# Performance work log

Hardware: AMD Instinct MI355X
Metric: run time of the kernel (lower is better)

Reference implementation:

```python
import jax, jax.numpy as jnp
import numpy as np

BS, NQ, NCLS = 16, 128, 3
T, P = 480, 72          # total targets, points per curve
COST_CLASS_W = 1.0
CURVES_W = 1.0
LOWER_W = 1.0
UPPER_W = 1.0


def setup_inputs() -> dict:
    key = jax.random.key(0)
    k1, k2, k3, k4, k5, k6, k7 = jax.random.split(key, 7)
    pred_logits = jax.random.normal(k1, (BS, NQ, NCLS), dtype=jnp.float32)
    pred_curves = jax.random.uniform(k2, (BS, NQ, 8), dtype=jnp.float32)
    # targets: [T, 5 + 2P] = [class_id, lower_y, upper_y, lower_x, upper_x, xs(P), ys(P)]
    ids = jax.random.randint(k3, (T,), 0, NCLS).astype(jnp.float32)
    ends = jax.random.uniform(k4, (T, 4), dtype=jnp.float32)  # ly, uy, lx, ux
    xs = jax.random.uniform(k5, (T, P), dtype=jnp.float32)
    ys = jax.random.uniform(k6, (T, P), dtype=jnp.float32)
    # variable number of valid points per lane; invalid points marked x = -1
    counts = jax.random.randint(k7, (T,), P // 2, P + 1)
    valid = jnp.arange(P)[None, :] < counts[:, None]
    xs = jnp.where(valid, xs, -1.0)
    targets = jnp.concatenate([ids[:, None], ends, xs, ys], axis=1)
    return {"pred_logits": pred_logits, "pred_curves": pred_curves, "targets": targets}


def reference(pred_logits, pred_curves, targets):
    bs, nq, _ = pred_logits.shape
    BN = bs * nq
    out_prob = jax.nn.softmax(pred_logits.reshape(BN, -1), axis=-1)
    tgt_ids = targets[:, 0].astype(jnp.int32)
    cost_class = -out_prob[:, tgt_ids]                      # [BN, T]

    ob = pred_curves.reshape(BN, 8)
    ly, uy, lx, ux = targets[:, 1], targets[:, 2], targets[:, 3], targets[:, 4]
    # L1 cdist on scalars == abs diff; averaged over (y, x) endpoint coords
    cost_lower = 0.5 * (jnp.abs(ob[:, 0:1] - ly[None, :]) + jnp.abs(ob[:, 2:3] - lx[None, :]))
    cost_upper = 0.5 * (jnp.abs(ob[:, 1:2] - uy[None, :]) + jnp.abs(ob[:, 3:4] - ux[None, :]))

    p = (targets.shape[1] - 5) // 2
    txs = targets[:, 5:5 + p]                               # [T, P]
    tys = targets[:, 5 + p:]                                # [T, P]
    valid = txs >= 0                                        # [T, P]
    per = jnp.sum(valid, axis=1).astype(jnp.float32)        # [T]
    total = jnp.sum(valid).astype(jnp.float32)
    w = jnp.sqrt(total / per)
    w = w / jnp.max(w)                                      # [T]

    p1 = jnp.stack([lx, ly], axis=-1)                       # [T, 2]
    p2 = jnp.stack([ux, uy], axis=-1)
    d = p2 - p1                                             # [T, 2]
    pi = jnp.stack([txs, tys], axis=-1)                     # [T, P, 2]
    p1pi = pi - p1[:, None, :]
    dot = jnp.einsum('tk,tpk->tp', d, p1pi)                 # [T, P]
    nrm = jnp.sqrt(jnp.sum(d * d, axis=-1))                 # [T]
    # original: proj = dot / nrm, then lam = proj / nrm
    lam = (dot / nrm[:, None]) / nrm[:, None]               # [T, P]

    a3, a2 = ob[:, 4], ob[:, 5]
    a1 = ob[:, 3] - a3 - a2 - ob[:, 2]
    a0 = ob[:, 2]
    b3, b2 = ob[:, 6], ob[:, 7]
    b1 = ob[:, 1] - b3 - b2 - ob[:, 0]
    b0 = ob[:, 0]

    L = lam[:, :, None]                                     # [T, P, 1] broadcast vs [BN]
    L2 = L * L
    L3 = L2 * L
    ox = a3 * L3 + a2 * L2 + a1 * L + a0                    # [T, P, BN]
    oy = b3 * L3 + b2 * L2 + b1 * L + b0

    diff = (txs[:, :, None] - ox) ** 2 + (tys[:, :, None] - oy) ** 2
    cost_polys = jnp.sum(jnp.where(valid[:, :, None], diff, 0.0), axis=1)  # [T, BN]
    cost_polys = cost_polys.T * w[None, :]                  # [BN, T]

    C = (COST_CLASS_W * cost_class + CURVES_W * cost_polys / 10.0
         + LOWER_W * cost_lower + UPPER_W * cost_upper)
    return C.reshape(bs, nq, -1)
```

## Files before the change

### kernel.cpp

```cpp
#include <hip/hip_runtime.h>
#include <math.h>

#define BS   16
#define NQ   128
#define NCLS 3
#define T    480
#define P    72
#define BN   (BS * NQ)
#define TROW (5 + 2 * P)
#define BNB  4

#define MD_OFF_B 0
#define EF_OFF_B 61440

__global__ __launch_bounds__(64) void moments_kernel(const float* __restrict__ targets,
                                                     double* __restrict__ MD,
                                                     float* __restrict__ EF) {
    int t    = blockIdx.x;
    int lane = threadIdx.x;
    const float* row = targets + (size_t)t * TROW;
    float ly = row[1], uy = row[2], lx = row[3], ux = row[4];
    float dx = ux - lx, dy = uy - ly;
    float nrm = sqrtf(dx * dx + dy * dy);

    double v[17];
#pragma unroll
    for (int i = 0; i < 17; ++i) v[i] = 0.0;

    for (int p = lane; p < P; p += 64) {
        float tx = row[5 + p];
        float ty = row[5 + P + p];
        if (tx >= 0.0f) {
            float lamf = dx * (tx - lx) + dy * (ty - ly);
            lamf = lamf / nrm / nrm;
            double L   = (double)lamf;
            double txd = (double)tx, tyd = (double)ty;
            double lp = 1.0;
#pragma unroll
            for (int j = 0; j < 7; ++j) {
                v[j] += lp;
                if (j < 4) {
                    v[7 + j]  += txd * lp;
                    v[11 + j] += tyd * lp;
                }
                lp *= L;
            }
            v[15] += txd * txd + tyd * tyd;
            v[16] += 1.0;
        }
    }

#pragma unroll
    for (int off = 32; off > 0; off >>= 1) {
#pragma unroll
        for (int i = 0; i < 17; ++i) v[i] += __shfl_down(v[i], off);
    }

    if (lane == 0) {
#pragma unroll
        for (int j = 0; j < 7; ++j) MD[j * T + t] = v[j];
#pragma unroll
        for (int k = 0; k < 4; ++k) {
            MD[(7 + k) * T + t]  = -2.0 * v[7 + k];
            MD[(11 + k) * T + t] = -2.0 * v[11 + k];
        }
        MD[15 * T + t] = v[15];
        EF[0 * T + t] = ly;
        EF[1 * T + t] = uy;
        EF[2 * T + t] = lx;
        EF[3 * T + t] = ux;
        EF[4 * T + t] = (float)v[16];
        EF[5 * T + t] = row[0];
    }
}

__global__ __launch_bounds__(512) void cost_kernel(const float* __restrict__ logits,
                                                   const float* __restrict__ curves,
                                                   const double* __restrict__ MD,
                                                   const float* __restrict__ EF,
                                                   float* __restrict__ out) {
    __shared__ float wavemin[8];
    int t    = threadIdx.x;
    int bn0  = blockIdx.x * BNB;
    int lane = t & 63;
    int wid  = t >> 6;

    float per = (t < T) ? EF[4 * T + t] : 1e30f;
    float pm = per;
#pragma unroll
    for (int off = 32; off > 0; off >>= 1) pm = fminf(pm, __shfl_xor(pm, off));
    if (lane == 0) wavemin[wid] = pm;
    __syncthreads();
    float per_min = wavemin[0];
#pragma unroll
    for (int i = 1; i < 8; ++i) per_min = fminf(per_min, wavemin[i]);

    if (t >= T) return;
    float w = sqrtf(per_min / per);

    double m[16];
#pragma unroll
    for (int r = 0; r < 16; ++r) m[r] = MD[r * T + t];
    float ly = EF[0 * T + t], uy = EF[1 * T + t];
    float lx = EF[2 * T + t], ux = EF[3 * T + t];
    int   id = (int)EF[5 * T + t];

#pragma unroll
    for (int j = 0; j < BNB; ++j) {
        int bn = bn0 + j;
        const float* ob = curves + (size_t)bn * 8;
        float o0 = ob[0], o1 = ob[1], o2 = ob[2], o3 = ob[3];
        float o4 = ob[4], o5 = ob[5], o6 = ob[6], o7 = ob[7];
        float a0 = o2, a1 = o3 - o4 - o5 - o2, a2 = o5, a3 = o4;
        float b0 = o0, b1 = o1 - o6 - o7 - o0, b2 = o7, b3 = o6;

        double A0 = a0, A1 = a1, A2 = a2, A3 = a3;
        double B0 = b0, B1 = b1, B2 = b2, B3 = b3;
        double acc = m[15]
            + (A0 * A0 + B0 * B0) * m[0]
            + 2.0 * (A0 * A1 + B0 * B1) * m[1]
            + (2.0 * (A0 * A2 + B0 * B2) + A1 * A1 + B1 * B1) * m[2]
            + 2.0 * (A0 * A3 + A1 * A2 + B0 * B3 + B1 * B2) * m[3]
            + (2.0 * (A1 * A3 + B1 * B3) + A2 * A2 + B2 * B2) * m[4]
            + 2.0 * (A2 * A3 + B2 * B3) * m[5]
            + (A3 * A3 + B3 * B3) * m[6]
            + A0 * m[7]  + A1 * m[8]  + A2 * m[9]  + A3 * m[10]
            + B0 * m[11] + B1 * m[12] + B2 * m[13] + B3 * m[14];

        const float* lg = logits + (size_t)bn * NCLS;
        float l0 = lg[0], l1 = lg[1], l2 = lg[2];
        float mx = fmaxf(l0, fmaxf(l1, l2));
        float e0 = __expf(l0 - mx), e1 = __expf(l1 - mx), e2 = __expf(l2 - mx);
        float inv = 1.0f / (e0 + e1 + e2);
        float prob = (id == 0) ? e0 * inv : ((id == 1) ? e1 * inv : e2 * inv);

        float cp = (float)acc * w * 0.1f;
        float cl = 0.5f * (fabsf(b0 - ly) + fabsf(a0 - lx));
        float cu = 0.5f * (fabsf(o1 - uy) + fabsf(o3 - ux));
        out[(size_t)bn * T + t] = -prob + cp + cl + cu;
    }
}

extern "C" void kernel_launch(void* const* d_in, const int* in_sizes, int n_in,
                              void* d_out, int out_size, void* d_ws, size_t ws_size,
                              hipStream_t stream) {
    const float* logits  = (const float*)d_in[0];
    const float* curves  = (const float*)d_in[1];
    const float* targets = (const float*)d_in[2];
    float* out = (float*)d_out;
    char*  ws  = (char*)d_ws;

    double* MD = (double*)(ws + MD_OFF_B);
    float*  EF = (float*) (ws + EF_OFF_B);

    moments_kernel<<<T, 64, 0, stream>>>(targets, MD, EF);
    cost_kernel<<<BN / BNB, 512, 0, stream>>>(logits, curves, MD, EF, out);
}
```

Baseline: 66.84 us.

## Fuse moments and cost kernels into one cooperative launch with grid sync

```diff
diff --git a/kernel.cpp b/kernel.cpp
--- a/kernel.cpp
+++ b/kernel.cpp
@@ -1,5 +1,8 @@
 #include <hip/hip_runtime.h>
+#include <hip/hip_cooperative_groups.h>
 #include <math.h>
+
+namespace cg = cooperative_groups;
 
 #define BS   16
 #define NQ   128
@@ -8,82 +11,87 @@
 #define P    72
 #define BN   (BS * NQ)
 #define TROW (5 + 2 * P)
-#define BNB  4
+#define NBLK 256
+#define NTHR 512
+#define BNB  (BN / NBLK)
 
 #define MD_OFF_B 0
 #define EF_OFF_B 61440
 
-__global__ __launch_bounds__(64) void moments_kernel(const float* __restrict__ targets,
-                                                     double* __restrict__ MD,
-                                                     float* __restrict__ EF) {
-    int t    = blockIdx.x;
-    int lane = threadIdx.x;
-    const float* row = targets + (size_t)t * TROW;
-    float ly = row[1], uy = row[2], lx = row[3], ux = row[4];
-    float dx = ux - lx, dy = uy - ly;
-    float nrm = sqrtf(dx * dx + dy * dy);
+__global__ __launch_bounds__(NTHR, 2) void fused_kernel(const float* __restrict__ logits,
+                                                        const float* __restrict__ curves,
+                                                        const float* __restrict__ targets,
+                                                        double* __restrict__ MD,
+                                                        float* __restrict__ EF,
+                                                        float* __restrict__ out) {
+    __shared__ float wavemin[NTHR / 64];
+    int tid  = threadIdx.x;
+    int lane = tid & 63;
+    int wid  = tid >> 6;
+    int g    = blockIdx.x * (NTHR / 64) + wid;
 
-    double v[17];
+    if (g < T) {
+        int t = g;
+        const float* row = targets + (size_t)t * TROW;
+        float ly = row[1], uy = row[2], lx = row[3], ux = row[4];
+        float dx = ux - lx, dy = uy - ly;
+        float nrm = sqrtf(dx * dx + dy * dy);
+
+        double v[17];
 #pragma unroll
-    for (int i = 0; i < 17; ++i) v[i] = 0.0;
+        for (int i = 0; i < 17; ++i) v[i] = 0.0;
 
-    for (int p = lane; p < P; p += 64) {
-        float tx = row[5 + p];
-        float ty = row[5 + P + p];
-        if (tx >= 0.0f) {
-            float lamf = dx * (tx - lx) + dy * (ty - ly);
-            lamf = lamf / nrm / nrm;
-            double L   = (double)lamf;
-            double txd = (double)tx, tyd = (double)ty;
-            double lp = 1.0;
+        for (int p = lane; p < P; p += 64) {
+            float tx = row[5 + p];
+            float ty = row[5 + P + p];
+            if (tx >= 0.0f) {
+                float lamf = dx * (tx - lx) + dy * (ty - ly);
+                lamf = lamf / nrm / nrm;
+                double L   = (double)lamf;
+                double txd = (double)tx, tyd = (double)ty;
+                double lp = 1.0;
 #pragma unroll
-            for (int j = 0; j < 7; ++j) {
-                v[j] += lp;
-                if (j < 4) {
-                    v[7 + j]  += txd * lp;
-                    v[11 + j] += tyd * lp;
+                for (int j = 0; j < 7; ++j) {
+                    v[j] += lp;
+                    if (j < 4) {
+                        v[7 + j]  += txd * lp;
+                        v[11 + j] += tyd * lp;
+                    }
+                    lp *= L;
                 }
-                lp *= L;
+                v[15] += txd * txd + tyd * tyd;
+                v[16] += 1.0;
             }
-            v[15] += txd * txd + tyd * tyd;
-            v[16] += 1.0;
+        }
+
+#pragma unroll
+        for (int off = 32; off > 0; off >>= 1) {
+#pragma unroll
+            for (int i = 0; i < 17; ++i) v[i] += __shfl_down(v[i], off);
+        }
+
+        if (lane == 0) {
+#pragma unroll
+            for (int j = 0; j < 7; ++j) MD[j * T + t] = v[j];
+#pragma unroll
+            for (int k = 0; k < 4; ++k) {
+                MD[(7 + k) * T + t]  = -2.0 * v[7 + k];
+                MD[(11 + k) * T + t] = -2.0 * v[11 + k];
+            }
+            MD[15 * T + t] = v[15];
+            EF[0 * T + t] = ly;
+            EF[1 * T + t] = uy;
+            EF[2 * T + t] = lx;
+            EF[3 * T + t] = ux;
+            EF[4 * T + t] = (float)v[16];
+            EF[5 * T + t] = row[0];
         }
     }
 
-#pragma unroll
-    for (int off = 32; off > 0; off >>= 1) {
-#pragma unroll
-        for (int i = 0; i < 17; ++i) v[i] += __shfl_down(v[i], off);
-    }
+    cg::this_grid().sync();
 
-    if (lane == 0) {
-#pragma unroll
-        for (int j = 0; j < 7; ++j) MD[j * T + t] = v[j];
-#pragma unroll
-        for (int k = 0; k < 4; ++k) {
-            MD[(7 + k) * T + t]  = -2.0 * v[7 + k];
-            MD[(11 + k) * T + t] = -2.0 * v[11 + k];
-        }
-        MD[15 * T + t] = v[15];
-        EF[0 * T + t] = ly;
-        EF[1 * T + t] = uy;
-        EF[2 * T + t] = lx;
-        EF[3 * T + t] = ux;
-        EF[4 * T + t] = (float)v[16];
-        EF[5 * T + t] = row[0];
-    }
-}
-
-__global__ __launch_bounds__(512) void cost_kernel(const float* __restrict__ logits,
-                                                   const float* __restrict__ curves,
-                                                   const double* __restrict__ MD,
-                                                   const float* __restrict__ EF,
-                                                   float* __restrict__ out) {
-    __shared__ float wavemin[8];
-    int t    = threadIdx.x;
-    int bn0  = blockIdx.x * BNB;
-    int lane = t & 63;
-    int wid  = t >> 6;
+    int t   = tid;
+    int bn0 = blockIdx.x * BNB;
 
     float per = (t < T) ? EF[4 * T + t] : 1e30f;
     float pm = per;
@@ -93,7 +101,7 @@
     __syncthreads();
     float per_min = wavemin[0];
 #pragma unroll
-    for (int i = 1; i < 8; ++i) per_min = fminf(per_min, wavemin[i]);
+    for (int i = 1; i < NTHR / 64; ++i) per_min = fminf(per_min, wavemin[i]);
 
     if (t >= T) return;
     float w = sqrtf(per_min / per);
@@ -153,6 +161,8 @@
     double* MD = (double*)(ws + MD_OFF_B);
     float*  EF = (float*) (ws + EF_OFF_B);
 
-    moments_kernel<<<T, 64, 0, stream>>>(targets, MD, EF);
-    cost_kernel<<<BN / BNB, 512, 0, stream>>>(logits, curves, MD, EF, out);
+    void* args[] = { (void*)&logits, (void*)&curves, (void*)&targets,
+                     (void*)&MD, (void*)&EF, (void*)&out };
+    hipLaunchCooperativeKernel((void*)fused_kernel, dim3(NBLK), dim3(NTHR),
+                               args, 0, stream);
 }
```

After: 103.7 us. +55.2%, slower.
